# Kernel optimization log

Hardware: AMD Instinct MI355X
Metric: run time of the kernel (lower is better)

Reference implementation:

```python
import jax, jax.numpy as jnp
import numpy as np
import math

E = 1024   # embedding_dim
H = 16     # num_attention_heads
DH = 64    # head_embedding_dim
THD = H * DH
EPS = 1e-5

def _layernorm(x, g, b):
    m = jnp.mean(x, axis=-1, keepdims=True)
    v = jnp.mean(jnp.square(x - m), axis=-1, keepdims=True)
    return (x - m) * jax.lax.rsqrt(v + EPS) * g + b

def setup_inputs() -> dict:
    key = jax.random.key(0)
    ks = jax.random.split(key, 16)
    s_in = 1.0 / math.sqrt(E)
    s_o = 1.0 / math.sqrt(THD)
    inp = {"tokens": jax.random.normal(ks[0], (2, 2048, E), dtype=jnp.float32)}
    # q_linear / k_linear / v_linear: LayerNorm(E) then Linear(E -> THD)
    for i, name in enumerate(["q", "k", "v"]):
        inp[f"ln_{name}_g"] = jnp.ones((E,), jnp.float32)
        inp[f"ln_{name}_b"] = jnp.zeros((E,), jnp.float32)
        inp[f"W{name}"] = jax.random.uniform(ks[1 + 2 * i], (E, THD), jnp.float32, -s_in, s_in)
        inp[f"b{name}"] = jax.random.uniform(ks[2 + 2 * i], (THD,), jnp.float32, -s_in, s_in)
    # attention_linear: LayerNorm(THD) then Linear(THD -> E)
    inp["ln_o_g"] = jnp.ones((THD,), jnp.float32)
    inp["ln_o_b"] = jnp.zeros((THD,), jnp.float32)
    inp["Wo"] = jax.random.uniform(ks[7], (THD, E), jnp.float32, -s_o, s_o)
    inp["bo"] = jax.random.uniform(ks[8], (E,), jnp.float32, -s_o, s_o)
    return inp

def reference(tokens, ln_q_g, ln_q_b, Wq, bq, ln_k_g, ln_k_b, Wk, bk,
              ln_v_g, ln_v_b, Wv, bv, ln_o_g, ln_o_b, Wo, bo):
    N, L, _ = tokens.shape
    # NOTE: faithful to source quirk -- k comes from v_linear, v comes from k_linear.
    q = (_layernorm(tokens, ln_q_g, ln_q_b) @ Wq + bq).reshape(N, L, H, DH).transpose(0, 2, 1, 3)  # (N,H,L,Dh)
    k = (_layernorm(tokens, ln_v_g, ln_v_b) @ Wv + bv).reshape(N, L, H, DH).transpose(0, 2, 3, 1)  # (N,H,Dh,L)
    v = (_layernorm(tokens, ln_k_g, ln_k_b) @ Wk + bk).reshape(N, L, H, DH).transpose(0, 2, 1, 3)  # (N,H,L,Dh)
    qkT = jnp.einsum('bhid,bhdj->bhij', q, k)  # (N,H,L,L)
    # mask added BEFORE dividing by sqrt(Dh), as in source
    mask = jnp.triu(jnp.full((L, L), -9999.0, dtype=qkT.dtype), k=1)
    attn = jax.nn.softmax((qkT + mask) / math.sqrt(DH), axis=-1)
    wv = jnp.einsum('bhij,bhjd->bhid', attn, v).transpose(0, 2, 1, 3).reshape(N, L, THD)
    out = _layernorm(wv, ln_o_g, ln_o_b) @ Wo + bo + tokens
    return (out, k, v)
```

## Files before the change

### kernel.cpp

```cpp
#include <hip/hip_runtime.h>

#define L_SEQ 2048
#define NH    16
#define E_DIM 1024
#define M_ROWS 4096

typedef unsigned short u16;
typedef unsigned int   u32;
typedef __attribute__((ext_vector_type(8))) __bf16 bf16x8;
typedef __attribute__((ext_vector_type(4))) float  f32x4;

__device__ __forceinline__ u16 f2bf(float f) {
  union { float f; u32 u; } x; x.f = f;
  u32 u = x.u;
  return (u16)((u + 0x7FFFu + ((u >> 16) & 1u)) >> 16);
}
__device__ __forceinline__ float bf2f(u16 v) {
  union { u32 u; float f; } x; x.u = ((u32)v) << 16;
  return x.f;
}
__device__ __forceinline__ void st_bf4(u16* p, float a, float b, float c, float d) {
  ushort4 u; u.x = f2bf(a); u.y = f2bf(b); u.z = f2bf(c); u.w = f2bf(d);
  *reinterpret_cast<ushort4*>(p) = u;
}
__device__ __forceinline__ void gload16(const u16* g, u16* l) {
  __builtin_amdgcn_global_load_lds(
      (const __attribute__((address_space(1))) void*)g,
      (__attribute__((address_space(3))) void*)l, 16, 0, 0);
}
#define SBAR() asm volatile("s_barrier" ::: "memory")

__global__ __launch_bounds__(256) void ln_hat_f32(const float* __restrict__ x, u16* __restrict__ o)
{
  __shared__ float red[8];
  const size_t row = blockIdx.x;
  const int t = threadIdx.x;
  float4 v = reinterpret_cast<const float4*>(x + row * E_DIM)[t];
  float s = v.x + v.y + v.z + v.w;
  float q = v.x*v.x + v.y*v.y + v.z*v.z + v.w*v.w;
  #pragma unroll
  for (int off = 32; off; off >>= 1) { s += __shfl_down(s, off); q += __shfl_down(q, off); }
  if ((t & 63) == 0) { red[t >> 6] = s; red[4 + (t >> 6)] = q; }
  __syncthreads();
  float S = red[0] + red[1] + red[2] + red[3];
  float Q = red[4] + red[5] + red[6] + red[7];
  float mean = S * (1.f / E_DIM);
  float rstd = rsqrtf(Q * (1.f / E_DIM) - mean * mean + 1e-5f);
  st_bf4(o + row * E_DIM + t * 4,
         (v.x - mean) * rstd, (v.y - mean) * rstd, (v.z - mean) * rstd, (v.w - mean) * rstd);
}

__global__ __launch_bounds__(256) void ln_hat_bf16(const u16* __restrict__ x, u16* __restrict__ o)
{
  __shared__ float red[8];
  const size_t row = blockIdx.x;
  const int t = threadIdx.x;
  ushort4 u = reinterpret_cast<const ushort4*>(x + row * E_DIM)[t];
  float v0 = bf2f(u.x), v1 = bf2f(u.y), v2 = bf2f(u.z), v3 = bf2f(u.w);
  float s = v0 + v1 + v2 + v3;
  float q = v0*v0 + v1*v1 + v2*v2 + v3*v3;
  #pragma unroll
  for (int off = 32; off; off >>= 1) { s += __shfl_down(s, off); q += __shfl_down(q, off); }
  if ((t & 63) == 0) { red[t >> 6] = s; red[4 + (t >> 6)] = q; }
  __syncthreads();
  float S = red[0] + red[1] + red[2] + red[3];
  float Q = red[4] + red[5] + red[6] + red[7];
  float mean = S * (1.f / E_DIM);
  float rstd = rsqrtf(Q * (1.f / E_DIM) - mean * mean + 1e-5f);
  st_bf4(o + row * E_DIM + t * 4,
         (v0 - mean) * rstd, (v1 - mean) * rstd, (v2 - mean) * rstd, (v3 - mean) * rstd);
}

__global__ __launch_bounds__(256) void transpose_all(
    const float* __restrict__ W0, const float* __restrict__ W1,
    const float* __restrict__ W2, const float* __restrict__ W3,
    const float* __restrict__ g0, const float* __restrict__ g1,
    const float* __restrict__ g2, const float* __restrict__ g3,
    u16* __restrict__ T0, u16* __restrict__ T1, u16* __restrict__ T2, u16* __restrict__ T3)
{
  __shared__ float tile[32][33];
  const int z = blockIdx.z;
  const float* W = (z == 0) ? W0 : (z == 1) ? W1 : (z == 2) ? W2 : W3;
  const float* g = (z == 0) ? g0 : (z == 1) ? g1 : (z == 2) ? g2 : g3;
  u16* T = (z == 0) ? T0 : (z == 1) ? T1 : (z == 2) ? T2 : T3;
  const int tx = threadIdx.x & 31, ty = threadIdx.x >> 5;
  const int bx = blockIdx.x * 32, by = blockIdx.y * 32;
  #pragma unroll
  for (int r = 0; r < 4; ++r) {
    const int e = by + ty + r * 8;
    tile[ty + r * 8][tx] = W[(size_t)e * E_DIM + bx + tx] * g[e];
  }
  __syncthreads();
  #pragma unroll
  for (int r = 0; r < 4; ++r)
    T[(size_t)(bx + ty + r * 8) * E_DIM + by + tx] = f2bf(tile[tx][ty + r * 8]);
}

__global__ __launch_bounds__(256) void bias_fold(
    const float* __restrict__ W0, const float* __restrict__ W1,
    const float* __restrict__ W2, const float* __restrict__ W3,
    const float* __restrict__ l0, const float* __restrict__ l1,
    const float* __restrict__ l2, const float* __restrict__ l3,
    const float* __restrict__ b0, const float* __restrict__ b1,
    const float* __restrict__ b2, const float* __restrict__ b3,
    float* __restrict__ bfold)
{
  __shared__ float part[8][32];
  const int z = blockIdx.y;
  const float* W  = (z == 0) ? W0 : (z == 1) ? W1 : (z == 2) ? W2 : W3;
  const float* bl = (z == 0) ? l0 : (z == 1) ? l1 : (z == 2) ? l2 : l3;
  const float* bs = (z == 0) ? b0 : (z == 1) ? b1 : (z == 2) ? b2 : b3;
  const int tn = threadIdx.x & 31, te = threadIdx.x >> 5;
  const int n = blockIdx.x * 32 + tn;
  float acc = 0.f;
  const int e0 = te * 128;
  for (int e = e0; e < e0 + 128; ++e) acc += bl[e] * W[(size_t)e * E_DIM + n];
  part[te][tn] = acc;
  __syncthreads();
  if (te == 0) {
    float s = part[0][tn] + part[1][tn] + part[2][tn] + part[3][tn]
            + part[4][tn] + part[5][tn] + part[6][tn] + part[7][tn];
    bfold[z * E_DIM + n] = bs[n] + s;
  }
}

#define GBK 64
__device__ __forceinline__ void core128(
    const u16* __restrict__ A, const u16* __restrict__ BT,
    int m0, int n0, int t, u16* lds, f32x4 (&acc)[4][4])
{
  const int lane = t & 63, wave = t >> 6;
  const int wm = wave >> 1, wn = wave & 1;
  const int fr = lane & 15, hi = lane >> 4;
  const int sx = fr & 7;

  auto STAGE = [&](int buf, int kt) {
    u16* la = lds + (buf * 2 + 0) * (128 * GBK);
    u16* lb = lds + (buf * 2 + 1) * (128 * GBK);
    #pragma unroll
    for (int s = 0; s < 4; ++s) {
      const int seg = t + s * 256;
      const int r = seg >> 3;
      const int gc = (seg & 7) ^ (r & 7);
      gload16(A + (size_t)(m0 + r) * E_DIM + kt * GBK + gc * 8, la + seg * 8);
    }
    #pragma unroll
    for (int s = 0; s < 4; ++s) {
      const int seg = t + s * 256;
      const int r = seg >> 3;
      const int gc = (seg & 7) ^ (r & 7);
      gload16(BT + (size_t)(n0 + r) * E_DIM + kt * GBK + gc * 8, lb + seg * 8);
    }
  };
  auto AF = [&](int buf, int i, int ks) -> bf16x8 {
    return *reinterpret_cast<const bf16x8*>(
        lds + (buf * 2 + 0) * (128 * GBK) + (wm * 64 + i * 16 + fr) * GBK + (((ks * 4 + hi) ^ sx) * 8));
  };
  auto BF = [&](int buf, int j, int ks) -> bf16x8 {
    return *reinterpret_cast<const bf16x8*>(
        lds + (buf * 2 + 1) * (128 * GBK) + (wn * 64 + j * 16 + fr) * GBK + (((ks * 4 + hi) ^ sx) * 8));
  };
  auto PHASES = [&](int buf) {
    bf16x8 a[4][2], b[4][2];
    #pragma unroll
    for (int i = 0; i < 4; ++i) { a[i][0] = AF(buf, i, 0); a[i][1] = AF(buf, i, 1); }
    #pragma unroll
    for (int j = 0; j < 4; ++j) { b[j][0] = BF(buf, j, 0); b[j][1] = BF(buf, j, 1); }
    __builtin_amdgcn_s_setprio(1);
    #pragma unroll
    for (int i = 0; i < 4; ++i)
      #pragma unroll
      for (int j = 0; j < 4; ++j) {
        acc[i][j] = __builtin_amdgcn_mfma_f32_16x16x32_bf16(a[i][0], b[j][0], acc[i][j], 0, 0, 0);
        acc[i][j] = __builtin_amdgcn_mfma_f32_16x16x32_bf16(a[i][1], b[j][1], acc[i][j], 0, 0, 0);
      }
    __builtin_amdgcn_s_setprio(0);
  };

  STAGE(0, 0);
  #pragma unroll 1
  for (int kt = 0; kt < 15; ++kt) {
    const int buf = kt & 1;
    SBAR();
    STAGE(buf ^ 1, kt + 1);
    asm volatile("s_waitcnt vmcnt(8)" ::: "memory");
    SBAR();
    PHASES(buf);
  }
  asm volatile("s_waitcnt vmcnt(0)" ::: "memory");
  SBAR();
  PHASES(1);
}

__global__ __launch_bounds__(256, 2) void gemm_qkv128(
    const u16* __restrict__ xhat, const u16* __restrict__ WTcat,
    const float* __restrict__ bfold,
    float* __restrict__ kout, float* __restrict__ vout,
    u16* __restrict__ qbf, u16* __restrict__ kbf, u16* __restrict__ vTb)
{
  __shared__ __align__(16) char smraw[128 * 132 * 4];
  u16* lds = (u16*)smraw;
  const int t = threadIdx.x;
  const int xcd = blockIdx.x & 7, l = blockIdx.x >> 3;
  const int by = 8 * (xcd >> 1) + l / 12;
  const int bx = 12 * (xcd & 1) + l % 12;
  const int m0 = by * 128, n0 = bx * 128;

  f32x4 acc[4][4] = {};
  core128(xhat, WTcat, m0, n0, t, lds, acc);

  const int lane = t & 63, wave = t >> 6;
  const int wm = wave >> 1, wn = wave & 1;
  const int fr = lane & 15, hi = lane >> 4;
  const int z = n0 >> 10;
  const float* bias = bfold + z * E_DIM;
  const int rowb = hi * 4;
  const int bb = m0 >> 11;

  if (z == 0) {
    #pragma unroll
    for (int i = 0; i < 4; ++i) {
      const int mbase = m0 + wm * 64 + i * 16 + rowb;
      #pragma unroll
      for (int j = 0; j < 4; ++j) {
        const int ncol = (n0 + wn * 64 + j * 16 + fr) & 1023;
        const float bval = bias[ncol];
        const int h = ncol >> 6, d = ncol & 63;
        #pragma unroll
        for (int r = 0; r < 4; ++r) {
          const int m = mbase + r;
          const int ltok = m & 2047;
          qbf[(((size_t)(bb * NH + h) * L_SEQ + ltok) << 6) + d] = f2bf(acc[i][j][r] + bval);
        }
      }
    }
  } else if (z == 1) {
    __syncthreads();
    float (*xp)[132] = (float(*)[132])smraw;
    #pragma unroll
    for (int i = 0; i < 4; ++i) {
      const int mbase = m0 + wm * 64 + i * 16 + rowb;
      const int mloc = wm * 64 + i * 16 + rowb;
      #pragma unroll
      for (int j = 0; j < 4; ++j) {
        const int nl = wn * 64 + j * 16 + fr;
        const int ncol = (n0 + nl) & 1023;
        const float bval = bias[ncol];
        const int h = ncol >> 6, d = ncol & 63;
        #pragma unroll
        for (int r = 0; r < 4; ++r) {
          const int m = mbase + r;
          const int ltok = m & 2047;
          const float val = acc[i][j][r] + bval;
          kbf[(((size_t)(bb * NH + h) * L_SEQ + ltok) << 6) + d] = f2bf(val);
          xp[nl][mloc + r] = val;
        }
      }
    }
    __syncthreads();
    const int nl = t >> 1, mh = (t & 1) * 64;
    const int ncol2 = (n0 + nl) & 1023;
    const int h2 = ncol2 >> 6, d2 = ncol2 & 63;
    float4* dst = (float4*)(kout + ((size_t)(bb * NH + h2) * 64 + d2) * L_SEQ + (m0 & 2047) + mh);
    #pragma unroll
    for (int u = 0; u < 16; ++u)
      dst[u] = *reinterpret_cast<float4*>(&xp[nl][mh + u * 4]);
  } else {
    __syncthreads();
    u32 (*vp)[68] = (u32(*)[68])smraw;
    #pragma unroll
    for (int i = 0; i < 4; ++i) {
      const int mbase = m0 + wm * 64 + i * 16 + rowb;
      const int mloc = wm * 64 + i * 16 + rowb;
      #pragma unroll
      for (int j = 0; j < 4; ++j) {
        const int nl = wn * 64 + j * 16 + fr;
        const int ncol = (n0 + nl) & 1023;
        const float bval = bias[ncol];
        const int h = ncol >> 6, d = ncol & 63;
        float v4[4];
        #pragma unroll
        for (int r = 0; r < 4; ++r) {
          const int m = mbase + r;
          const int ltok = m & 2047;
          v4[r] = acc[i][j][r] + bval;
          vout[((size_t)(bb * NH + h) * L_SEQ + ltok) * 64 + d] = v4[r];
        }
        vp[nl][(mloc >> 1) + 0] = (u32)f2bf(v4[0]) | ((u32)f2bf(v4[1]) << 16);
        vp[nl][(mloc >> 1) + 1] = (u32)f2bf(v4[2]) | ((u32)f2bf(v4[3]) << 16);
      }
    }
    __syncthreads();
    const int nl = t >> 1, mh = (t & 1) * 64;
    const int ncol2 = (n0 + nl) & 1023;
    const int h2 = ncol2 >> 6, d2 = ncol2 & 63;
    uint4* dst = (uint4*)(vTb + ((size_t)(bb * NH + h2) * 64 + d2) * L_SEQ + (m0 & 2047) + mh);
    #pragma unroll
    for (int u = 0; u < 8; ++u)
      dst[u] = *reinterpret_cast<uint4*>(&vp[nl][(mh >> 1) + u * 4]);
  }
}

__global__ __launch_bounds__(256, 2) void gemm_o128(
    const u16* __restrict__ A, const u16* __restrict__ BT, const float* __restrict__ bias,
    const float* __restrict__ tokens, float* __restrict__ out)
{
  __shared__ u16 lds[4 * 128 * GBK];
  const int t = threadIdx.x;
  const int xcd = blockIdx.x & 7, l = blockIdx.x >> 3;
  const int by = 8 * (xcd >> 1) + (l >> 2);
  const int bx = 4 * (xcd & 1) + (l & 3);
  const int m0 = by * 128, n0 = bx * 128;

  f32x4 acc[4][4] = {};
  core128(A, BT, m0, n0, t, lds, acc);

  const int lane = t & 63, wave = t >> 6;
  const int wm = wave >> 1, wn = wave & 1;
  const int fr = lane & 15, hi = lane >> 4;
  const int rowb = hi * 4;
  #pragma unroll
  for (int i = 0; i < 4; ++i) {
    const int mbase = m0 + wm * 64 + i * 16 + rowb;
    #pragma unroll
    for (int j = 0; j < 4; ++j) {
      const int ncol = n0 + wn * 64 + j * 16 + fr;
      const float bval = bias[ncol];
      #pragma unroll
      for (int r = 0; r < 4; ++r) {
        const int m = mbase + r;
        out[(size_t)m * E_DIM + ncol] = acc[i][j][r] + bval + tokens[(size_t)m * E_DIM + ncol];
      }
    }
  }
}

__global__ __launch_bounds__(256, 4) void attn_split(
    const u16* __restrict__ qbf, const u16* __restrict__ kbf,
    const u16* __restrict__ vTb, u16* __restrict__ wv,
    float* __restrict__ po, float* __restrict__ pml)
{
  __shared__ u16 Klds[64][72];
  __shared__ u16 Vlds[64][72];
  __shared__ u16 Plds[4][16][72];
  const int t = threadIdx.x, lane = t & 63, wave = t >> 6;
  const int bi = blockIdx.x;
  const int bh = (bi & 7) + 8 * ((bi >> 3) & 3);
  const int pp = bi >> 5;
  const int half = pp & 1, pr = pp >> 1;
  const int fr = lane & 15, hi = lane >> 4;
  const u16* kbase = kbf + (size_t)bh * L_SEQ * 64;
  const u16* vbase = vTb + (size_t)bh * 64 * L_SEQ;
  const int b = bh >> 4, h = bh & 15;
  const int qtA = 31 - pr, qtB = pr;

  auto STG = [&](int j0) {
    #pragma unroll
    for (int s = 0; s < 2; ++s) {
      const int seg = t + s * 256;
      const int r = seg >> 3, c8 = (seg & 7) * 8;
      *reinterpret_cast<uint4*>(&Klds[r][c8]) =
          *reinterpret_cast<const uint4*>(kbase + (size_t)(j0 + r) * 64 + c8);
      *reinterpret_cast<uint4*>(&Vlds[r][c8]) =
          *reinterpret_cast<const uint4*>(vbase + (size_t)r * L_SEQ + j0 + c8);
    }
  };
  auto TILE = [&](const bf16x8& qf0, const bf16x8& qf1, int qg, bool diag, int j0,
                  f32x4 (&o)[4], float& mrun, float& lrun) {
    f32x4 st[4] = {};
    __builtin_amdgcn_s_setprio(1);
    #pragma unroll
    for (int kt = 0; kt < 4; ++kt) {
      bf16x8 ka0 = *reinterpret_cast<const bf16x8*>(&Klds[kt*16 + fr][hi*8]);
      bf16x8 ka1 = *reinterpret_cast<const bf16x8*>(&Klds[kt*16 + fr][32 + hi*8]);
      st[kt] = __builtin_amdgcn_mfma_f32_16x16x32_bf16(ka0, qf0, st[kt], 0, 0, 0);
      st[kt] = __builtin_amdgcn_mfma_f32_16x16x32_bf16(ka1, qf1, st[kt], 0, 0, 0);
    }
    __builtin_amdgcn_s_setprio(0);

    float p[16];
    float pmax = -3.0e38f;
    #pragma unroll
    for (int kt = 0; kt < 4; ++kt)
      #pragma unroll
      for (int r = 0; r < 4; ++r) {
        const int key = j0 + kt*16 + hi*4 + r;
        const float v = st[kt][r] * 0.125f + ((diag && key > qg) ? -1249.875f : 0.f);
        p[kt*4 + r] = v;
        pmax = fmaxf(pmax, v);
      }
    pmax = fmaxf(pmax, __shfl_xor(pmax, 16));
    pmax = fmaxf(pmax, __shfl_xor(pmax, 32));
    const float mnew = fmaxf(mrun, pmax);
    const float alpha = __expf(mrun - mnew);
    float lsum = 0.f;
    #pragma unroll
    for (int i = 0; i < 16; ++i) { p[i] = __expf(p[i] - mnew); lsum += p[i]; }
    lsum += __shfl_xor(lsum, 16);
    lsum += __shfl_xor(lsum, 32);
    lrun = lrun * alpha + lsum;
    mrun = mnew;
    #pragma unroll
    for (int r = 0; r < 4; ++r) {
      const float ar = __shfl(alpha, hi*4 + r);
      o[0][r] *= ar; o[1][r] *= ar; o[2][r] *= ar; o[3][r] *= ar;
    }
    #pragma unroll
    for (int kt = 0; kt < 4; ++kt) {
      ushort4 w4;
      w4.x = f2bf(p[kt*4+0]); w4.y = f2bf(p[kt*4+1]);
      w4.z = f2bf(p[kt*4+2]); w4.w = f2bf(p[kt*4+3]);
      *reinterpret_cast<ushort4*>(&Plds[wave][fr][kt*16 + hi*4]) = w4;
    }
    const bf16x8 pf0 = *reinterpret_cast<const bf16x8*>(&Plds[wave][fr][hi*8]);
    const bf16x8 pf1 = *reinterpret_cast<const bf16x8*>(&Plds[wave][fr][32 + hi*8]);
    __builtin_amdgcn_s_setprio(1);
    #pragma unroll
    for (int dt = 0; dt < 4; ++dt) {
      bf16x8 vf0 = *reinterpret_cast<const bf16x8*>(&Vlds[dt*16 + fr][hi*8]);
      bf16x8 vf1 = *reinterpret_cast<const bf16x8*>(&Vlds[dt*16 + fr][32 + hi*8]);
      o[dt] = __builtin_amdgcn_mfma_f32_16x16x32_bf16(pf0, vf0, o[dt], 0, 0, 0);
      o[dt] = __builtin_amdgcn_mfma_f32_16x16x32_bf16(pf1, vf1, o[dt], 0, 0, 0);
    }
    __builtin_amdgcn_s_setprio(0);
  };

  {
    const int q0w = qtA * 64 + wave * 16;
    const int qg = q0w + fr;
    const u16* qrow = qbf + ((size_t)bh * L_SEQ + q0w + fr) * 64 + hi * 8;
    const bf16x8 qf0 = *reinterpret_cast<const bf16x8*>(qrow);
    const bf16x8 qf1 = *reinterpret_cast<const bf16x8*>(qrow + 32);
    f32x4 o[4] = {};
    float mrun = -3.0e38f, lrun = 0.f;
    const int lo = half ? 17 : 0;
    const int hiT = half ? qtA : 16;
    #pragma unroll 1
    for (int tkv = lo; tkv <= hiT; ++tkv) {
      STG(tkv * 64);
      __syncthreads();
      TILE(qf0, qf1, qg, tkv == qtA, tkv * 64, o, mrun, lrun);
      __syncthreads();
    }
    const int slot = (bh * 16 + pr) * 2 + half;
    float* pob = po + (size_t)slot * 4096;
    #pragma unroll
    for (int dt = 0; dt < 4; ++dt)
      #pragma unroll
      for (int r = 0; r < 4; ++r)
        pob[(wave * 16 + hi * 4 + r) * 64 + dt * 16 + fr] = o[dt][r];
    if (hi == 0) {
      pml[slot * 128 + wave * 16 + fr] = mrun;
      pml[slot * 128 + 64 + wave * 16 + fr] = lrun;
    }
  }

  if (half) {
    const int q0w = qtB * 64 + wave * 16;
    const int qg = q0w + fr;
    const u16* qrow = qbf + ((size_t)bh * L_SEQ + q0w + fr) * 64 + hi * 8;
    const bf16x8 qf0 = *reinterpret_cast<const bf16x8*>(qrow);
    const bf16x8 qf1 = *reinterpret_cast<const bf16x8*>(qrow + 32);
    f32x4 o[4] = {};
    float mrun = -3.0e38f, lrun = 0.f;
    #pragma unroll 1
    for (int tkv = 0; tkv <= qtB; ++tkv) {
      __syncthreads();
      STG(tkv * 64);
      __syncthreads();
      TILE(qf0, qf1, qg, tkv == qtB, tkv * 64, o, mrun, lrun);
    }
    const float inv = 1.f / lrun;
    #pragma unroll
    for (int r = 0; r < 4; ++r) {
      const float ir = __shfl(inv, hi * 4 + r);
      const int q = q0w + hi * 4 + r;
      u16* dst = wv + (size_t)(b * L_SEQ + q) * E_DIM + h * 64 + fr;
      #pragma unroll
      for (int dt = 0; dt < 4; ++dt)
        dst[dt * 16] = f2bf(o[dt][r] * ir);
    }
  }
}

__global__ __launch_bounds__(256) void attn_combine(
    const float* __restrict__ po, const float* __restrict__ pml, u16* __restrict__ wv)
{
  const int pair = blockIdx.x;
  const int bh = pair >> 4, pr = pair & 15;
  const int b = bh >> 4, h = bh & 15;
  const int q0 = (31 - pr) * 64;
  const int t = threadIdx.x;
  const int r = t >> 2, c0 = (t & 3) * 16;
  const float m0 = pml[(size_t)(pair * 2 + 0) * 128 + r];
  const float l0 = pml[(size_t)(pair * 2 + 0) * 128 + 64 + r];
  const float m1 = pml[(size_t)(pair * 2 + 1) * 128 + r];
  const float l1 = pml[(size_t)(pair * 2 + 1) * 128 + 64 + r];
  const float mm = fmaxf(m0, m1);
  const float a0 = __expf(m0 - mm), a1 = __expf(m1 - mm);
  const float inv = 1.f / (l0 * a0 + l1 * a1);
  const float* o0 = po + ((size_t)(pair * 2 + 0) * 64 + r) * 64 + c0;
  const float* o1 = po + ((size_t)(pair * 2 + 1) * 64 + r) * 64 + c0;
  u16* dst = wv + (size_t)(b * L_SEQ + q0 + r) * E_DIM + h * 64 + c0;
  #pragma unroll
  for (int c = 0; c < 16; c += 4) {
    float4 x0 = *reinterpret_cast<const float4*>(o0 + c);
    float4 x1 = *reinterpret_cast<const float4*>(o1 + c);
    st_bf4(dst + c,
           (x0.x * a0 + x1.x * a1) * inv, (x0.y * a0 + x1.y * a1) * inv,
           (x0.z * a0 + x1.z * a1) * inv, (x0.w * a0 + x1.w * a1) * inv);
  }
}

__global__ __launch_bounds__(256) void attn_mfma(
    const u16* __restrict__ qbf, const u16* __restrict__ kbf,
    const u16* __restrict__ vTb, u16* __restrict__ wv)
{
  __shared__ u16 Klds[64][72];
  __shared__ u16 Vlds[64][72];
  __shared__ u16 Plds[4][16][72];
  const int t = threadIdx.x, lane = t & 63, wave = t >> 6;
  const int bi = blockIdx.x;
  const int bh = (bi & 7) + 8 * ((bi >> 3) & 3);
  const int pr = bi >> 5;
  const int fr = lane & 15, hi = lane >> 4;
  const u16* kbase = kbf + (size_t)bh * L_SEQ * 64;
  const u16* vbase = vTb + (size_t)bh * 64 * L_SEQ;
  const int b = bh >> 4, h = bh & 15;

  #pragma unroll 1
  for (int half = 0; half < 2; ++half) {
    const int qt = half ? (31 - pr) : pr;
    const int q0w = qt * 64 + wave * 16;
    const int qg = q0w + fr;
    const u16* qrow = qbf + ((size_t)bh * L_SEQ + q0w + fr) * 64 + hi * 8;
    const bf16x8 qf0 = *reinterpret_cast<const bf16x8*>(qrow);
    const bf16x8 qf1 = *reinterpret_cast<const bf16x8*>(qrow + 32);
    f32x4 o[4] = {};
    float mrun = -3.0e38f, lrun = 0.f;

    for (int tkv = 0; tkv <= qt; ++tkv) {
      const int j0 = tkv * 64;
      const bool diag = (tkv == qt);
      #pragma unroll
      for (int s = 0; s < 2; ++s) {
        const int seg = t + s * 256;
        const int r = seg >> 3, c8 = (seg & 7) * 8;
        *reinterpret_cast<uint4*>(&Klds[r][c8]) =
            *reinterpret_cast<const uint4*>(kbase + (size_t)(j0 + r) * 64 + c8);
        *reinterpret_cast<uint4*>(&Vlds[r][c8]) =
            *reinterpret_cast<const uint4*>(vbase + (size_t)r * L_SEQ + j0 + c8);
      }
      __syncthreads();

      f32x4 st[4] = {};
      __builtin_amdgcn_s_setprio(1);
      #pragma unroll
      for (int kt = 0; kt < 4; ++kt) {
        bf16x8 ka0 = *reinterpret_cast<const bf16x8*>(&Klds[kt*16 + fr][hi*8]);
        bf16x8 ka1 = *reinterpret_cast<const bf16x8*>(&Klds[kt*16 + fr][32 + hi*8]);
        st[kt] = __builtin_amdgcn_mfma_f32_16x16x32_bf16(ka0, qf0, st[kt], 0, 0, 0);
        st[kt] = __builtin_amdgcn_mfma_f32_16x16x32_bf16(ka1, qf1, st[kt], 0, 0, 0);
      }
      __builtin_amdgcn_s_setprio(0);

      float p[16];
      float pmax = -3.0e38f;
      #pragma unroll
      for (int kt = 0; kt < 4; ++kt)
        #pragma unroll
        for (int r = 0; r < 4; ++r) {
          const int key = j0 + kt*16 + hi*4 + r;
          const float v = st[kt][r] * 0.125f + ((diag && key > qg) ? -1249.875f : 0.f);
          p[kt*4 + r] = v;
          pmax = fmaxf(pmax, v);
        }
      pmax = fmaxf(pmax, __shfl_xor(pmax, 16));
      pmax = fmaxf(pmax, __shfl_xor(pmax, 32));
      const float mnew = fmaxf(mrun, pmax);
      const float alpha = __expf(mrun - mnew);
      float lsum = 0.f;
      #pragma unroll
      for (int i = 0; i < 16; ++i) { p[i] = __expf(p[i] - mnew); lsum += p[i]; }
      lsum += __shfl_xor(lsum, 16);
      lsum += __shfl_xor(lsum, 32);
      lrun = lrun * alpha + lsum;
      mrun = mnew;
      #pragma unroll
      for (int r = 0; r < 4; ++r) {
        const float ar = __shfl(alpha, hi*4 + r);
        o[0][r] *= ar; o[1][r] *= ar; o[2][r] *= ar; o[3][r] *= ar;
      }
      #pragma unroll
      for (int kt = 0; kt < 4; ++kt) {
        ushort4 w4;
        w4.x = f2bf(p[kt*4+0]); w4.y = f2bf(p[kt*4+1]);
        w4.z = f2bf(p[kt*4+2]); w4.w = f2bf(p[kt*4+3]);
        *reinterpret_cast<ushort4*>(&Plds[wave][fr][kt*16 + hi*4]) = w4;
      }
      const bf16x8 pf0 = *reinterpret_cast<const bf16x8*>(&Plds[wave][fr][hi*8]);
      const bf16x8 pf1 = *reinterpret_cast<const bf16x8*>(&Plds[wave][fr][32 + hi*8]);
      __builtin_amdgcn_s_setprio(1);
      #pragma unroll
      for (int dt = 0; dt < 4; ++dt) {
        bf16x8 vf0 = *reinterpret_cast<const bf16x8*>(&Vlds[dt*16 + fr][hi*8]);
        bf16x8 vf1 = *reinterpret_cast<const bf16x8*>(&Vlds[dt*16 + fr][32 + hi*8]);
        o[dt] = __builtin_amdgcn_mfma_f32_16x16x32_bf16(pf0, vf0, o[dt], 0, 0, 0);
        o[dt] = __builtin_amdgcn_mfma_f32_16x16x32_bf16(pf1, vf1, o[dt], 0, 0, 0);
      }
      __builtin_amdgcn_s_setprio(0);
      __syncthreads();
    }

    const float inv = 1.f / lrun;
    #pragma unroll
    for (int r = 0; r < 4; ++r) {
      const float ir = __shfl(inv, hi*4 + r);
      const int q = q0w + hi*4 + r;
      u16* dst = wv + (size_t)(b * L_SEQ + q) * E_DIM + h * 64 + fr;
      #pragma unroll
      for (int dt = 0; dt < 4; ++dt)
        dst[dt * 16] = f2bf(o[dt][r] * ir);
    }
  }
}

extern "C" void kernel_launch(void* const* d_in, const int* in_sizes, int n_in,
                              void* d_out, int out_size, void* d_ws, size_t ws_size,
                              hipStream_t stream) {
  (void)in_sizes; (void)n_in; (void)out_size;
  const float* tokens = (const float*)d_in[0];
  const float* ln_q_g = (const float*)d_in[1];
  const float* ln_q_b = (const float*)d_in[2];
  const float* Wq     = (const float*)d_in[3];
  const float* bq     = (const float*)d_in[4];
  const float* ln_k_g = (const float*)d_in[5];
  const float* ln_k_b = (const float*)d_in[6];
  const float* Wk     = (const float*)d_in[7];
  const float* bk     = (const float*)d_in[8];
  const float* ln_v_g = (const float*)d_in[9];
  const float* ln_v_b = (const float*)d_in[10];
  const float* Wv     = (const float*)d_in[11];
  const float* bv     = (const float*)d_in[12];
  const float* ln_o_g = (const float*)d_in[13];
  const float* ln_o_b = (const float*)d_in[14];
  const float* Wo     = (const float*)d_in[15];
  const float* bo     = (const float*)d_in[16];

  float* out  = (float*)d_out;
  float* kout = out + 4194304;
  float* vout = kout + 4194304;

  char* w = (char*)d_ws;
  const size_t MB = (size_t)1 << 20;
  u16*   WTq   = (u16*)(w + 0 * MB);
  u16*   WTv   = (u16*)(w + 2 * MB);
  u16*   WTk   = (u16*)(w + 4 * MB);
  u16*   WTo   = (u16*)(w + 6 * MB);
  u16*   xhat  = (u16*)(w + 8 * MB);
  u16*   qbf   = (u16*)(w + 16 * MB);
  u16*   kbf   = (u16*)(w + 24 * MB);
  u16*   vTb   = (u16*)(w + 32 * MB);
  u16*   what  = (u16*)(w + 40 * MB);
  float* bfold = (float*)(w + 48 * MB);
  float* po    = (float*)(w + 49 * MB);
  float* pml   = (float*)(w + 65 * MB);
  u16*   wvb   = xhat;

  transpose_all<<<dim3(32, 32, 4), 256, 0, stream>>>(
      Wq, Wv, Wk, Wo, ln_q_g, ln_v_g, ln_k_g, ln_o_g, WTq, WTv, WTk, WTo);
  bias_fold<<<dim3(32, 4), 256, 0, stream>>>(
      Wq, Wv, Wk, Wo, ln_q_b, ln_v_b, ln_k_b, ln_o_b, bq, bv, bk, bo, bfold);
  ln_hat_f32<<<M_ROWS, 256, 0, stream>>>(tokens, xhat);
  gemm_qkv128<<<768, 256, 0, stream>>>(xhat, WTq, bfold, kout, vout, qbf, kbf, vTb);
  if (ws_size >= 66 * MB) {
    attn_split<<<1024, 256, 0, stream>>>(qbf, kbf, vTb, wvb, po, pml);
    attn_combine<<<512, 256, 0, stream>>>(po, pml, wvb);
  } else {
    attn_mfma<<<512, 256, 0, stream>>>(qbf, kbf, vTb, wvb);
  }
  ln_hat_bf16<<<M_ROWS, 256, 0, stream>>>(wvb, what);
  gemm_o128<<<256, 256, 0, stream>>>(what, WTo, bfold + 3 * E_DIM, tokens, out);
}
```

Measured before the change: 129.5 us.

## Merge prep kernels into one launch and fuse split-attention combine with output LayerNorm

The weight transpose, bias fold and input LayerNorm kernels become one launch whose block index ranges pick the branch. The split-attention combine now runs inside the output LayerNorm kernel: for the query tiles that were split, each row merges the two partial results using their max/sum statistics before normalising. This saves several kernel launches and one round trip of the combined attention output through global memory. In exchange the prep kernel is a divergent multi-role grid, and the combine relies on the partial-buffer indexing matching attn_split.

```diff
diff --git a/kernel.cpp b/kernel.cpp
--- a/kernel.cpp
+++ b/kernel.cpp
@@ -30,24 +30,76 @@
 }
 #define SBAR() asm volatile("s_barrier" ::: "memory")
 
-__global__ __launch_bounds__(256) void ln_hat_f32(const float* __restrict__ x, u16* __restrict__ o)
-{
-  __shared__ float red[8];
-  const size_t row = blockIdx.x;
+__global__ __launch_bounds__(256) void prep_kernel(
+    const float* __restrict__ tokens,
+    const float* __restrict__ W0, const float* __restrict__ W1,
+    const float* __restrict__ W2, const float* __restrict__ W3,
+    const float* __restrict__ g0, const float* __restrict__ g1,
+    const float* __restrict__ g2, const float* __restrict__ g3,
+    const float* __restrict__ lb0, const float* __restrict__ lb1,
+    const float* __restrict__ lb2, const float* __restrict__ lb3,
+    const float* __restrict__ bs0, const float* __restrict__ bs1,
+    const float* __restrict__ bs2, const float* __restrict__ bs3,
+    u16* __restrict__ T0, u16* __restrict__ T1, u16* __restrict__ T2, u16* __restrict__ T3,
+    float* __restrict__ bfold, u16* __restrict__ xhat)
+{
+  __shared__ __align__(16) float shm[32 * 33];
+  const int bid = blockIdx.x;
   const int t = threadIdx.x;
-  float4 v = reinterpret_cast<const float4*>(x + row * E_DIM)[t];
-  float s = v.x + v.y + v.z + v.w;
-  float q = v.x*v.x + v.y*v.y + v.z*v.z + v.w*v.w;
-  #pragma unroll
-  for (int off = 32; off; off >>= 1) { s += __shfl_down(s, off); q += __shfl_down(q, off); }
-  if ((t & 63) == 0) { red[t >> 6] = s; red[4 + (t >> 6)] = q; }
-  __syncthreads();
-  float S = red[0] + red[1] + red[2] + red[3];
-  float Q = red[4] + red[5] + red[6] + red[7];
-  float mean = S * (1.f / E_DIM);
-  float rstd = rsqrtf(Q * (1.f / E_DIM) - mean * mean + 1e-5f);
-  st_bf4(o + row * E_DIM + t * 4,
-         (v.x - mean) * rstd, (v.y - mean) * rstd, (v.z - mean) * rstd, (v.w - mean) * rstd);
+
+  if (bid < 4096) {
+    const int z = bid >> 10, rem = bid & 1023;
+    const float* W = (z == 0) ? W0 : (z == 1) ? W1 : (z == 2) ? W2 : W3;
+    const float* g = (z == 0) ? g0 : (z == 1) ? g1 : (z == 2) ? g2 : g3;
+    u16* T = (z == 0) ? T0 : (z == 1) ? T1 : (z == 2) ? T2 : T3;
+    float (*tile)[33] = (float(*)[33])shm;
+    const int tx = t & 31, ty = t >> 5;
+    const int bx = (rem & 31) * 32, by = (rem >> 5) * 32;
+    #pragma unroll
+    for (int r = 0; r < 4; ++r) {
+      const int e = by + ty + r * 8;
+      tile[ty + r * 8][tx] = W[(size_t)e * E_DIM + bx + tx] * g[e];
+    }
+    __syncthreads();
+    #pragma unroll
+    for (int r = 0; r < 4; ++r)
+      T[(size_t)(bx + ty + r * 8) * E_DIM + by + tx] = f2bf(tile[tx][ty + r * 8]);
+  } else if (bid < 4224) {
+    const int idx = bid - 4096;
+    const int z = idx >> 5;
+    const float* W  = (z == 0) ? W0 : (z == 1) ? W1 : (z == 2) ? W2 : W3;
+    const float* bl = (z == 0) ? lb0 : (z == 1) ? lb1 : (z == 2) ? lb2 : lb3;
+    const float* bs = (z == 0) ? bs0 : (z == 1) ? bs1 : (z == 2) ? bs2 : bs3;
+    float (*part)[32] = (float(*)[32])shm;
+    const int tn = t & 31, te = t >> 5;
+    const int n = (idx & 31) * 32 + tn;
+    float acc = 0.f;
+    const int e0 = te * 128;
+    for (int e = e0; e < e0 + 128; ++e) acc += bl[e] * W[(size_t)e * E_DIM + n];
+    part[te][tn] = acc;
+    __syncthreads();
+    if (te == 0) {
+      float s = part[0][tn] + part[1][tn] + part[2][tn] + part[3][tn]
+              + part[4][tn] + part[5][tn] + part[6][tn] + part[7][tn];
+      bfold[z * E_DIM + n] = bs[n] + s;
+    }
+  } else {
+    float* red = shm;
+    const size_t row = bid - 4224;
+    float4 v = reinterpret_cast<const float4*>(tokens + row * E_DIM)[t];
+    float s = v.x + v.y + v.z + v.w;
+    float q = v.x*v.x + v.y*v.y + v.z*v.z + v.w*v.w;
+    #pragma unroll
+    for (int off = 32; off; off >>= 1) { s += __shfl_down(s, off); q += __shfl_down(q, off); }
+    if ((t & 63) == 0) { red[t >> 6] = s; red[4 + (t >> 6)] = q; }
+    __syncthreads();
+    float S = red[0] + red[1] + red[2] + red[3];
+    float Q = red[4] + red[5] + red[6] + red[7];
+    float mean = S * (1.f / E_DIM);
+    float rstd = rsqrtf(Q * (1.f / E_DIM) - mean * mean + 1e-5f);
+    st_bf4(xhat + row * E_DIM + t * 4,
+           (v.x - mean) * rstd, (v.y - mean) * rstd, (v.z - mean) * rstd, (v.w - mean) * rstd);
+  }
 }
 
 __global__ __launch_bounds__(256) void ln_hat_bf16(const u16* __restrict__ x, u16* __restrict__ o)
@@ -71,57 +123,52 @@
          (v0 - mean) * rstd, (v1 - mean) * rstd, (v2 - mean) * rstd, (v3 - mean) * rstd);
 }
 
-__global__ __launch_bounds__(256) void transpose_all(
-    const float* __restrict__ W0, const float* __restrict__ W1,
-    const float* __restrict__ W2, const float* __restrict__ W3,
-    const float* __restrict__ g0, const float* __restrict__ g1,
-    const float* __restrict__ g2, const float* __restrict__ g3,
-    u16* __restrict__ T0, u16* __restrict__ T1, u16* __restrict__ T2, u16* __restrict__ T3)
-{
-  __shared__ float tile[32][33];
-  const int z = blockIdx.z;
-  const float* W = (z == 0) ? W0 : (z == 1) ? W1 : (z == 2) ? W2 : W3;
-  const float* g = (z == 0) ? g0 : (z == 1) ? g1 : (z == 2) ? g2 : g3;
-  u16* T = (z == 0) ? T0 : (z == 1) ? T1 : (z == 2) ? T2 : T3;
-  const int tx = threadIdx.x & 31, ty = threadIdx.x >> 5;
-  const int bx = blockIdx.x * 32, by = blockIdx.y * 32;
+__global__ __launch_bounds__(256) void ln_combine_hat(
+    const u16* __restrict__ wvb, const float* __restrict__ po,
+    const float* __restrict__ pml, u16* __restrict__ what)
+{
+  __shared__ float red[8];
+  const int row = blockIdx.x;
+  const int t = threadIdx.x;
+  const int l = row & (L_SEQ - 1), b = row >> 11;
+  const int qt = l >> 6;
+  float v0, v1, v2, v3;
+  if (qt >= 16) {
+    const int pr = 31 - qt;
+    const int c = t * 4;
+    const int h = c >> 6, d0 = c & 63;
+    const int bh = b * NH + h;
+    const int base = (bh * 16 + pr) * 2;
+    const int rr = l & 63;
+    const float m0 = pml[(size_t)base * 128 + rr];
+    const float s0 = pml[(size_t)base * 128 + 64 + rr];
+    const float m1 = pml[(size_t)(base + 1) * 128 + rr];
+    const float s1 = pml[(size_t)(base + 1) * 128 + 64 + rr];
+    const float mm = fmaxf(m0, m1);
+    const float a0 = __expf(m0 - mm), a1 = __expf(m1 - mm);
+    const float inv = 1.f / (s0 * a0 + s1 * a1);
+    float4 x0 = *reinterpret_cast<const float4*>(po + ((size_t)base * 64 + rr) * 64 + d0);
+    float4 x1 = *reinterpret_cast<const float4*>(po + ((size_t)(base + 1) * 64 + rr) * 64 + d0);
+    v0 = (x0.x * a0 + x1.x * a1) * inv;
+    v1 = (x0.y * a0 + x1.y * a1) * inv;
+    v2 = (x0.z * a0 + x1.z * a1) * inv;
+    v3 = (x0.w * a0 + x1.w * a1) * inv;
+  } else {
+    ushort4 u = reinterpret_cast<const ushort4*>(wvb + (size_t)row * E_DIM)[t];
+    v0 = bf2f(u.x); v1 = bf2f(u.y); v2 = bf2f(u.z); v3 = bf2f(u.w);
+  }
+  float s = v0 + v1 + v2 + v3;
+  float q = v0*v0 + v1*v1 + v2*v2 + v3*v3;
   #pragma unroll
-  for (int r = 0; r < 4; ++r) {
-    const int e = by + ty + r * 8;
-    tile[ty + r * 8][tx] = W[(size_t)e * E_DIM + bx + tx] * g[e];
-  }
+  for (int off = 32; off; off >>= 1) { s += __shfl_down(s, off); q += __shfl_down(q, off); }
+  if ((t & 63) == 0) { red[t >> 6] = s; red[4 + (t >> 6)] = q; }
   __syncthreads();
-  #pragma unroll
-  for (int r = 0; r < 4; ++r)
-    T[(size_t)(bx + ty + r * 8) * E_DIM + by + tx] = f2bf(tile[tx][ty + r * 8]);
-}
-
-__global__ __launch_bounds__(256) void bias_fold(
-    const float* __restrict__ W0, const float* __restrict__ W1,
-    const float* __restrict__ W2, const float* __restrict__ W3,
-    const float* __restrict__ l0, const float* __restrict__ l1,
-    const float* __restrict__ l2, const float* __restrict__ l3,
-    const float* __restrict__ b0, const float* __restrict__ b1,
-    const float* __restrict__ b2, const float* __restrict__ b3,
-    float* __restrict__ bfold)
-{
-  __shared__ float part[8][32];
-  const int z = blockIdx.y;
-  const float* W  = (z == 0) ? W0 : (z == 1) ? W1 : (z == 2) ? W2 : W3;
-  const float* bl = (z == 0) ? l0 : (z == 1) ? l1 : (z == 2) ? l2 : l3;
-  const float* bs = (z == 0) ? b0 : (z == 1) ? b1 : (z == 2) ? b2 : b3;
-  const int tn = threadIdx.x & 31, te = threadIdx.x >> 5;
-  const int n = blockIdx.x * 32 + tn;
-  float acc = 0.f;
-  const int e0 = te * 128;
-  for (int e = e0; e < e0 + 128; ++e) acc += bl[e] * W[(size_t)e * E_DIM + n];
-  part[te][tn] = acc;
-  __syncthreads();
-  if (te == 0) {
-    float s = part[0][tn] + part[1][tn] + part[2][tn] + part[3][tn]
-            + part[4][tn] + part[5][tn] + part[6][tn] + part[7][tn];
-    bfold[z * E_DIM + n] = bs[n] + s;
-  }
+  float S = red[0] + red[1] + red[2] + red[3];
+  float Q = red[4] + red[5] + red[6] + red[7];
+  float mean = S * (1.f / E_DIM);
+  float rstd = rsqrtf(Q * (1.f / E_DIM) - mean * mean + 1e-5f);
+  st_bf4(what + (size_t)row * E_DIM + t * 4,
+         (v0 - mean) * rstd, (v1 - mean) * rstd, (v2 - mean) * rstd, (v3 - mean) * rstd);
 }
 
 #define GBK 64
@@ -667,18 +714,20 @@
   float* pml   = (float*)(w + 65 * MB);
   u16*   wvb   = xhat;
 
-  transpose_all<<<dim3(32, 32, 4), 256, 0, stream>>>(
-      Wq, Wv, Wk, Wo, ln_q_g, ln_v_g, ln_k_g, ln_o_g, WTq, WTv, WTk, WTo);
-  bias_fold<<<dim3(32, 4), 256, 0, stream>>>(
-      Wq, Wv, Wk, Wo, ln_q_b, ln_v_b, ln_k_b, ln_o_b, bq, bv, bk, bo, bfold);
-  ln_hat_f32<<<M_ROWS, 256, 0, stream>>>(tokens, xhat);
+  prep_kernel<<<8320, 256, 0, stream>>>(
+      tokens,
+      Wq, Wv, Wk, Wo,
+      ln_q_g, ln_v_g, ln_k_g, ln_o_g,
+      ln_q_b, ln_v_b, ln_k_b, ln_o_b,
+      bq, bv, bk, bo,
+      WTq, WTv, WTk, WTo, bfold, xhat);
   gemm_qkv128<<<768, 256, 0, stream>>>(xhat, WTq, bfold, kout, vout, qbf, kbf, vTb);
   if (ws_size >= 66 * MB) {
     attn_split<<<1024, 256, 0, stream>>>(qbf, kbf, vTb, wvb, po, pml);
-    attn_combine<<<512, 256, 0, stream>>>(po, pml, wvb);
+    ln_combine_hat<<<M_ROWS, 256, 0, stream>>>(wvb, po, pml, what);
   } else {
     attn_mfma<<<512, 256, 0, stream>>>(qbf, kbf, vTb, wvb);
-  }
-  ln_hat_bf16<<<M_ROWS, 256, 0, stream>>>(wvb, what);
+    ln_hat_bf16<<<M_ROWS, 256, 0, stream>>>(wvb, ln_o_g ? what : what);
+  }
   gemm_o128<<<256, 256, 0, stream>>>(what, WTo, bfold + 3 * E_DIM, tokens, out);
 }
```

Result: faster. 124.6 us (-3.7%).
